# Optimization experiments

Hardware: AMD Instinct MI355X
Metric: run time of the kernel (lower is better)

## Reference

```python
import jax, jax.numpy as jnp
import numpy as np

HID = 64
NUM_LAYER = 3
N_OBJ = 100000
N_P1, N_P2, N_P3 = 200000, 400000, 200000
NUM_GRAPHS = 256


def _mlp(x, w1, b1, w2, b2):
    # pyg.nn.MLP([in, hid, out], norm=None): Linear -> ReLU -> Linear
    return jnp.dot(jax.nn.relu(jnp.dot(x, w1) + b1), w2) + b2


def _gather(obj, ei):
    # ei: [arity, n_atoms] object index per argument slot
    r, n = ei.shape
    g = jnp.take(obj, ei, axis=0)  # [r, n, HID]
    return jnp.moveaxis(g, 0, 1).reshape(n, r * HID)  # concat per-position embeddings


def _scatter(atom, ei, n_obj):
    # split atom embedding [n, r*HID] into r chunks and scatter-add to objects
    r, n = ei.shape
    chunks = jnp.moveaxis(atom.reshape(n, r, HID), 1, 0).reshape(r * n, HID)
    return jax.ops.segment_sum(chunks, ei.reshape(-1), num_segments=n_obj)


def _lin_init(key, fan_in, fan_out):
    kw, kb = jax.random.split(key)
    w = jax.random.normal(kw, (fan_in, fan_out), jnp.float32) / np.float32(np.sqrt(fan_in))
    b = jax.random.normal(kb, (fan_out,), jnp.float32) * 0.01
    return w, b


def setup_inputs() -> dict:
    key = jax.random.key(0)
    ks = jax.random.split(key, 16)
    inp = {}
    inp["x_obj"] = jnp.zeros((N_OBJ, 1), jnp.float32)
    inp["x_p1"] = jnp.zeros((N_P1, 1), jnp.float32)
    inp["x_p2"] = jnp.zeros((N_P2, 2), jnp.float32)
    inp["x_p3"] = jnp.zeros((N_P3, 3), jnp.float32)
    for i, (name, r) in enumerate([("p1", 1), ("p2", 2), ("p3", 3)]):
        d = HID * r
        w1, b1 = _lin_init(ks[2 * i], d, d)
        w2, b2 = _lin_init(ks[2 * i + 1], d, d)
        inp[f"w_{name}_1"], inp[f"b_{name}_1"] = w1, b1
        inp[f"w_{name}_2"], inp[f"b_{name}_2"] = w2, b2
    inp["w_u1"], inp["b_u1"] = _lin_init(ks[6], 2 * HID, 2 * HID)
    inp["w_u2"], inp["b_u2"] = _lin_init(ks[7], 2 * HID, HID)
    inp["w_r1"], inp["b_r1"] = _lin_init(ks[8], HID, 2 * HID)
    inp["w_r2"], inp["b_r2"] = _lin_init(ks[9], 2 * HID, 1)
    inp["ei_p1"] = jax.random.randint(ks[10], (1, N_P1), 0, N_OBJ, jnp.int32)
    inp["ei_p2"] = jax.random.randint(ks[11], (2, N_P2), 0, N_OBJ, jnp.int32)
    inp["ei_p3"] = jax.random.randint(ks[12], (3, N_P3), 0, N_OBJ, jnp.int32)
    inp["batch_obj"] = jnp.sort(jax.random.randint(ks[13], (N_OBJ,), 0, NUM_GRAPHS, jnp.int32))
    inp["num_graphs"] = NUM_GRAPHS
    return inp


def reference(x_obj, x_p1, x_p2, x_p3,
              w_p1_1, b_p1_1, w_p1_2, b_p1_2,
              w_p2_1, b_p2_1, w_p2_2, b_p2_2,
              w_p3_1, b_p3_1, w_p3_2, b_p3_2,
              w_u1, b_u1, w_u2, b_u2,
              w_r1, b_r1, w_r2, b_r2,
              ei_p1, ei_p2, ei_p3, batch_obj, num_graphs):
    n_obj = x_obj.shape[0]
    # encoding_layer: everything starts at zeros of size [N, F*hidden]
    obj = jnp.zeros((n_obj, x_obj.shape[1] * HID), jnp.float32)
    for _ in range(NUM_LAYER):
        # FanOutMP: gather arg-object embeddings, per-predicate MLP -> atom embeddings
        a1 = _mlp(_gather(obj, ei_p1), w_p1_1, b_p1_1, w_p1_2, b_p1_2)
        a2 = _mlp(_gather(obj, ei_p2), w_p2_1, b_p2_1, w_p2_2, b_p2_2)
        a3 = _mlp(_gather(obj, ei_p3), w_p3_1, b_p3_1, w_p3_2, b_p3_2)
        # FanInMP: split atom emb into arity chunks, scatter-add back to objects
        agg = (_scatter(a1, ei_p1, n_obj) + _scatter(a2, ei_p2, n_obj)
               + _scatter(a3, ei_p3, n_obj))
        # obj_update on cat([old_obj, aggregated])
        obj = _mlp(jnp.concatenate([obj, agg], axis=1), w_u1, b_u1, w_u2, b_u2)
    # global_add_pool + readout
    pooled = jax.ops.segment_sum(obj, batch_obj, num_segments=num_graphs)
    return _mlp(pooled, w_r1, b_r1, w_r2, b_r2).reshape(-1)
```

## Files before the change

### kernel.cpp

```cpp
#include <hip/hip_runtime.h>

typedef _Float16 h8 __attribute__((ext_vector_type(8)));
typedef _Float16 h4 __attribute__((ext_vector_type(4)));
typedef float f32x4 __attribute__((ext_vector_type(4)));

__device__ __forceinline__ f32x4 mfma3(h8 ah, h8 al, h8 bh, h8 bl, f32x4 c) {
    c = __builtin_amdgcn_mfma_f32_16x16x32_f16(ah, bh, c, 0, 0, 0);
    c = __builtin_amdgcn_mfma_f32_16x16x32_f16(ah, bl, c, 0, 0, 0);
    c = __builtin_amdgcn_mfma_f32_16x16x32_f16(al, bh, c, 0, 0, 0);
    return c;
}

__launch_bounds__(256)
__global__ void wprep(const float* __restrict__ w_p1_1, const float* __restrict__ w_p1_2,
                      const float* __restrict__ w_p2_1, const float* __restrict__ w_p2_2,
                      const float* __restrict__ w_p3_1, const float* __restrict__ w_p3_2,
                      const float* __restrict__ w_u1, const float* __restrict__ w_u2,
                      _Float16* __restrict__ hb)
{
    int b = blockIdx.x;
    const float* src; int K, N, base; size_t off;
    if      (b < 16)  { src = w_p1_1; K = 64;  N = 64;  base = 0;   off = 0;      }
    else if (b < 32)  { src = w_p1_2; K = 64;  N = 64;  base = 16;  off = 8192;   }
    else if (b < 96)  { src = w_p2_1; K = 128; N = 128; base = 32;  off = 16384;  }
    else if (b < 160) { src = w_p2_2; K = 128; N = 128; base = 96;  off = 49152;  }
    else if (b < 304) { src = w_p3_1; K = 192; N = 192; base = 160; off = 81920;  }
    else if (b < 448) { src = w_p3_2; K = 192; N = 192; base = 304; off = 155648; }
    else if (b < 512) { src = w_u1;   K = 128; N = 128; base = 448; off = 229376; }
    else              { src = w_u2;   K = 128; N = 64;  base = 512; off = 262144; }
    int e = (b - base) * 256 + threadIdx.x;
    if (e < K * N) {
        int n = e / K, k = e - n * K;
        float x = src[k * N + n];
        _Float16 h = (_Float16)x;
        hb[off + e] = h;
        hb[off + (size_t)K * N + e] = (_Float16)(x - (float)h);
    }
}

__launch_bounds__(256)
__global__ void aconst_k(const float* __restrict__ b_p1_1, const float* __restrict__ w_p1_2,
                         const float* __restrict__ b_p1_2,
                         const float* __restrict__ b_p2_1, const float* __restrict__ w_p2_2,
                         const float* __restrict__ b_p2_2,
                         const float* __restrict__ b_p3_1, const float* __restrict__ w_p3_2,
                         const float* __restrict__ b_p3_2,
                         float* __restrict__ ac)
{
    int p = blockIdx.x;
    const float *b1, *w2, *b2; int D, off;
    if      (p == 0) { b1 = b_p1_1; w2 = w_p1_2; b2 = b_p1_2; D = 64;  off = 0;   }
    else if (p == 1) { b1 = b_p2_1; w2 = w_p2_2; b2 = b_p2_2; D = 128; off = 64;  }
    else             { b1 = b_p3_1; w2 = w_p3_2; b2 = b_p3_2; D = 192; off = 192; }
    int n = threadIdx.x;
    if (n < D) {
        float s = b2[n];
        for (int k = 0; k < D; ++k) {
            float h = b1[k];
            h = h > 0.f ? h : 0.f;
            s = fmaf(h, w2[k * D + n], s);
        }
        ac[off + n] = s;
    }
}

__launch_bounds__(256)
__global__ void hist_k(const int* __restrict__ ei1, const int* __restrict__ ei2,
                       const int* __restrict__ ei3, int* __restrict__ counts,
                       int n_obj, int n1, int n2, int n3)
{
    int e = blockIdx.x * 256 + threadIdx.x;
    int t1 = n1, t2 = n1 + 2 * n2, t3 = t2 + 3 * n3;
    if (e < t1) {
        atomicAdd(&counts[ei1[e]], 1);
    } else if (e < t2) {
        int x = e - t1; int slot = x / n2;
        atomicAdd(&counts[(size_t)(1 + slot) * n_obj + ei2[x]], 1);
    } else if (e < t3) {
        int x = e - t2; int slot = x / n3;
        atomicAdd(&counts[(size_t)(3 + slot) * n_obj + ei3[x]], 1);
    }
}

__launch_bounds__(256)
__global__ void bcast_k(const int* __restrict__ counts, const float* __restrict__ ac,
                        float* __restrict__ agg, int n_obj)
{
    __shared__ float ch[384];
    int tid = threadIdx.x;
    for (int i = tid; i < 384; i += 256) ch[i] = ac[i];
    __syncthreads();
    int i = blockIdx.x * 256 + tid;
    int o = i >> 4, q = i & 15;
    if (o < n_obj) {
        float c[6];
#pragma unroll
        for (int j = 0; j < 6; ++j) c[j] = (float)counts[(size_t)j * n_obj + o];
        float4 v;
        float* vp = (float*)&v;
#pragma unroll
        for (int comp = 0; comp < 4; ++comp) {
            int col = 4 * q + comp;
            float s = 0.f;
#pragma unroll
            for (int j = 0; j < 6; ++j) s = fmaf(c[j], ch[j * 64 + col], s);
            vp[comp] = s;
        }
        ((float4*)agg)[(size_t)o * 16 + q] = v;
    }
}

template<int R>
__device__ __forceinline__ void pred_body(
    char* smem,
    const float* __restrict__ obj, const int* __restrict__ ei,
    const _Float16* __restrict__ W1h, const _Float16* __restrict__ W1l,
    const float* __restrict__ B1,
    const _Float16* __restrict__ W2h, const _Float16* __restrict__ W2l,
    const float* __restrict__ B2,
    float* __restrict__ agg, int n_atoms, int blk)
{
    constexpr int D = 64 * R;
    constexpr int KC = D / 32;
    constexpr int LDA = D + 8;
    _Float16* Ah = (_Float16*)smem;
    _Float16* Al = Ah + 64 * LDA;
    int* eis = (int*)(Al + 64 * LDA);

    const int tid = threadIdx.x;
    const int wave = tid >> 6, lane = tid & 63;
    const int r = lane & 15, g = lane >> 4;
    const int a_base = blk * 64;
    const int tb = wave * R;

    for (int i = tid; i < R * 64; i += 256) {
        int s = i >> 6, a = i & 63;
        int ag = a_base + a; if (ag >= n_atoms) ag = n_atoms - 1;
        eis[i] = ei[s * n_atoms + ag];
    }
    __syncthreads();
    {
        const float4* obj4 = (const float4*)obj;
        float4 vv[4 * R];
#pragma unroll
        for (int i = 0; i < 4 * R; ++i) {
            int f = tid + 256 * i;
            int a = f / (R * 16), rem = f % (R * 16);
            int s = rem >> 4, q = rem & 15;
            vv[i] = obj4[(size_t)eis[s * 64 + a] * 16 + q];
        }
#pragma unroll
        for (int i = 0; i < 4 * R; ++i) {
            int f = tid + 256 * i;
            int a = f / (R * 16), rem = f % (R * 16);
            int s = rem >> 4, q = rem & 15;
            float4 v = vv[i];
            _Float16 h0 = (_Float16)v.x, h1 = (_Float16)v.y,
                     h2 = (_Float16)v.z, h3 = (_Float16)v.w;
            h4 hv = {h0, h1, h2, h3};
            h4 lv = {(_Float16)(v.x - (float)h0), (_Float16)(v.y - (float)h1),
                     (_Float16)(v.z - (float)h2), (_Float16)(v.w - (float)h3)};
            *(h4*)(Ah + a * LDA + s * 64 + 4 * q) = hv;
            *(h4*)(Al + a * LDA + s * 64 + 4 * q) = lv;
        }
    }
    __syncthreads();

    f32x4 z = {0.f, 0.f, 0.f, 0.f};
    f32x4 acc[4][R];
#pragma unroll
    for (int rt = 0; rt < 4; ++rt)
#pragma unroll
        for (int t = 0; t < R; ++t) acc[rt][t] = z;

    {
        h8 bh[2][R], bl[2][R];
#pragma unroll
        for (int t = 0; t < R; ++t) {
            size_t wo = (size_t)((tb + t) * 16 + r) * D + g * 8;
            bh[0][t] = *(const h8*)(W1h + wo);
            bl[0][t] = *(const h8*)(W1l + wo);
        }
#pragma unroll
        for (int kc = 0; kc < KC; ++kc) {
            const int cur = kc & 1, nxt = cur ^ 1;
            if (kc + 1 < KC) {
#pragma unroll
                for (int t = 0; t < R; ++t) {
                    size_t wo = (size_t)((tb + t) * 16 + r) * D + (kc + 1) * 32 + g * 8;
                    bh[nxt][t] = *(const h8*)(W1h + wo);
                    bl[nxt][t] = *(const h8*)(W1l + wo);
                }
            }
            const int ko = kc * 32 + g * 8;
            h8 ah[4], al[4];
#pragma unroll
            for (int rt = 0; rt < 4; ++rt) {
                ah[rt] = *(const h8*)(Ah + (rt * 16 + r) * LDA + ko);
                al[rt] = *(const h8*)(Al + (rt * 16 + r) * LDA + ko);
            }
#pragma unroll
            for (int t = 0; t < R; ++t)
#pragma unroll
                for (int rt = 0; rt < 4; ++rt)
                    acc[rt][t] = mfma3(ah[rt], al[rt], bh[cur][t], bl[cur][t], acc[rt][t]);
        }
    }
    __syncthreads();

#pragma unroll
    for (int t = 0; t < R; ++t) {
        int col = (tb + t) * 16 + r;
        float b1 = B1[col];
#pragma unroll
        for (int rt = 0; rt < 4; ++rt)
#pragma unroll
            for (int q = 0; q < 4; ++q) {
                int row = rt * 16 + g * 4 + q;
                float h = acc[rt][t][q] + b1;
                h = h > 0.f ? h : 0.f;
                _Float16 hh = (_Float16)h;
                Ah[row * LDA + col] = hh;
                Al[row * LDA + col] = (_Float16)(h - (float)hh);
            }
    }
    __syncthreads();

#pragma unroll
    for (int rt = 0; rt < 4; ++rt)
#pragma unroll
        for (int t = 0; t < R; ++t) acc[rt][t] = z;
    {
        h8 bh[2][R], bl[2][R];
#pragma unroll
        for (int t = 0; t < R; ++t) {
            size_t wo = (size_t)((tb + t) * 16 + r) * D + g * 8;
            bh[0][t] = *(const h8*)(W2h + wo);
            bl[0][t] = *(const h8*)(W2l + wo);
        }
#pragma unroll
        for (int kc = 0; kc < KC; ++kc) {
            const int cur = kc & 1, nxt = cur ^ 1;
            if (kc + 1 < KC) {
#pragma unroll
                for (int t = 0; t < R; ++t) {
                    size_t wo = (size_t)((tb + t) * 16 + r) * D + (kc + 1) * 32 + g * 8;
                    bh[nxt][t] = *(const h8*)(W2h + wo);
                    bl[nxt][t] = *(const h8*)(W2l + wo);
                }
            }
            const int ko = kc * 32 + g * 8;
            h8 ah[4], al[4];
#pragma unroll
            for (int rt = 0; rt < 4; ++rt) {
                ah[rt] = *(const h8*)(Ah + (rt * 16 + r) * LDA + ko);
                al[rt] = *(const h8*)(Al + (rt * 16 + r) * LDA + ko);
            }
#pragma unroll
            for (int t = 0; t < R; ++t)
#pragma unroll
                for (int rt = 0; rt < 4; ++rt)
                    acc[rt][t] = mfma3(ah[rt], al[rt], bh[cur][t], bl[cur][t], acc[rt][t]);
        }
    }

#pragma unroll
    for (int t = 0; t < R; ++t) {
        int col = (tb + t) * 16 + r;
        float b2 = B2[col];
        int s = col >> 6, cc = col & 63;
#pragma unroll
        for (int rt = 0; rt < 4; ++rt)
#pragma unroll
            for (int q = 0; q < 4; ++q) {
                int row = rt * 16 + g * 4 + q;
                int atom = a_base + row;
                if (atom < n_atoms)
                    atomicAdd(agg + (size_t)eis[s * 64 + row] * 64 + cc,
                              acc[rt][t][q] + b2);
            }
    }
}

__launch_bounds__(256, 3)
__global__ void pred_all(const float* __restrict__ obj, float* __restrict__ agg,
                         const int* __restrict__ ei1, const int* __restrict__ ei2,
                         const int* __restrict__ ei3,
                         const _Float16* __restrict__ hb,
                         const float* __restrict__ b_p1_1, const float* __restrict__ b_p1_2,
                         const float* __restrict__ b_p2_1, const float* __restrict__ b_p2_2,
                         const float* __restrict__ b_p3_1, const float* __restrict__ b_p3_2,
                         int n1, int n2, int n3, int nb3, int nb2)
{
    extern __shared__ char smem[];
    int b = blockIdx.x;
    if (b < nb3) {
        pred_body<3>(smem, obj, ei3, hb + 81920, hb + 118784, b_p3_1,
                     hb + 155648, hb + 192512, b_p3_2, agg, n3, b);
    } else if (b < nb3 + nb2) {
        pred_body<2>(smem, obj, ei2, hb + 16384, hb + 32768, b_p2_1,
                     hb + 49152, hb + 65536, b_p2_2, agg, n2, b - nb3);
    } else {
        pred_body<1>(smem, obj, ei1, hb + 0, hb + 4096, b_p1_1,
                     hb + 8192, hb + 12288, b_p1_2, agg, n1, b - nb3 - nb2);
    }
}

template<int FIRST>
__launch_bounds__(256, 4)
__global__ void update_mfma(float* __restrict__ obj, float* __restrict__ agg,
                            const _Float16* __restrict__ W1h, const _Float16* __restrict__ W1l,
                            const float* __restrict__ B1,
                            const _Float16* __restrict__ W2h, const _Float16* __restrict__ W2l,
                            const float* __restrict__ B2,
                            int n_obj, int zero_agg)
{
    constexpr int LDA = 136;
    __shared__ _Float16 Ah[64 * LDA];
    __shared__ _Float16 Al[64 * LDA];

    const int tid = threadIdx.x;
    const int wave = tid >> 6, lane = tid & 63;
    const int r = lane & 15, g = lane >> 4;
    const int a_base = blockIdx.x * 64;

    {
        const float4* o4 = (const float4*)obj;
        const float4* g4 = (const float4*)agg;
#pragma unroll
        for (int i = 0; i < 8; ++i) {
            int f = tid + 256 * i;
            int a = f >> 5, q = f & 31;
            int rg = a_base + a; if (rg >= n_obj) rg = n_obj - 1;
            float4 v;
            if (FIRST && q < 16) {
                v = make_float4(0.f, 0.f, 0.f, 0.f);
            } else {
                v = (q < 16) ? o4[(size_t)rg * 16 + q] : g4[(size_t)rg * 16 + (q - 16)];
            }
            _Float16 h0 = (_Float16)v.x, h1 = (_Float16)v.y,
                     h2 = (_Float16)v.z, h3 = (_Float16)v.w;
            h4 hv = {h0, h1, h2, h3};
            h4 lv = {(_Float16)(v.x - (float)h0), (_Float16)(v.y - (float)h1),
                     (_Float16)(v.z - (float)h2), (_Float16)(v.w - (float)h3)};
            *(h4*)(Ah + a * LDA + 4 * q) = hv;
            *(h4*)(Al + a * LDA + 4 * q) = lv;
        }
    }
    __syncthreads();

    f32x4 z = {0.f, 0.f, 0.f, 0.f};
    f32x4 acc[4][2];
#pragma unroll
    for (int rt = 0; rt < 4; ++rt) { acc[rt][0] = z; acc[rt][1] = z; }
    {
        h8 bh[2][2], bl[2][2];
#pragma unroll
        for (int t = 0; t < 2; ++t) {
            size_t wo = (size_t)((wave * 2 + t) * 16 + r) * 128 + g * 8;
            bh[0][t] = *(const h8*)(W1h + wo);
            bl[0][t] = *(const h8*)(W1l + wo);
        }
#pragma unroll
        for (int kc = 0; kc < 4; ++kc) {
            const int cur = kc & 1, nxt = cur ^ 1;
            if (kc + 1 < 4) {
#pragma unroll
                for (int t = 0; t < 2; ++t) {
                    size_t wo = (size_t)((wave * 2 + t) * 16 + r) * 128 + (kc + 1) * 32 + g * 8;
                    bh[nxt][t] = *(const h8*)(W1h + wo);
                    bl[nxt][t] = *(const h8*)(W1l + wo);
                }
            }
            const int ko = kc * 32 + g * 8;
            h8 ah[4], al[4];
#pragma unroll
            for (int rt = 0; rt < 4; ++rt) {
                ah[rt] = *(const h8*)(Ah + (rt * 16 + r) * LDA + ko);
                al[rt] = *(const h8*)(Al + (rt * 16 + r) * LDA + ko);
            }
#pragma unroll
            for (int t = 0; t < 2; ++t)
#pragma unroll
                for (int rt = 0; rt < 4; ++rt)
                    acc[rt][t] = mfma3(ah[rt], al[rt], bh[cur][t], bl[cur][t], acc[rt][t]);
        }
    }
    __syncthreads();
#pragma unroll
    for (int t = 0; t < 2; ++t) {
        int col = (wave * 2 + t) * 16 + r;
        float b1 = B1[col];
#pragma unroll
        for (int rt = 0; rt < 4; ++rt)
#pragma unroll
            for (int q = 0; q < 4; ++q) {
                int row = rt * 16 + g * 4 + q;
                float h = acc[rt][t][q] + b1;
                h = h > 0.f ? h : 0.f;
                _Float16 hh = (_Float16)h;
                Ah[row * LDA + col] = hh;
                Al[row * LDA + col] = (_Float16)(h - (float)hh);
            }
    }
    __syncthreads();

    f32x4 acc2[4];
#pragma unroll
    for (int rt = 0; rt < 4; ++rt) acc2[rt] = z;
    {
        h8 bh[2], bl[2];
        {
            size_t wo = (size_t)(wave * 16 + r) * 128 + g * 8;
            bh[0] = *(const h8*)(W2h + wo);
            bl[0] = *(const h8*)(W2l + wo);
        }
#pragma unroll
        for (int kc = 0; kc < 4; ++kc) {
            const int cur = kc & 1, nxt = cur ^ 1;
            if (kc + 1 < 4) {
                size_t wo = (size_t)(wave * 16 + r) * 128 + (kc + 1) * 32 + g * 8;
                bh[nxt] = *(const h8*)(W2h + wo);
                bl[nxt] = *(const h8*)(W2l + wo);
            }
            const int ko = kc * 32 + g * 8;
#pragma unroll
            for (int rt = 0; rt < 4; ++rt) {
                h8 ah = *(const h8*)(Ah + (rt * 16 + r) * LDA + ko);
                h8 al = *(const h8*)(Al + (rt * 16 + r) * LDA + ko);
                acc2[rt] = mfma3(ah, al, bh[cur], bl[cur], acc2[rt]);
            }
        }
    }
    {
        int col = wave * 16 + r;
        float b2 = B2[col];
#pragma unroll
        for (int rt = 0; rt < 4; ++rt)
#pragma unroll
            for (int q = 0; q < 4; ++q) {
                int row = a_base + rt * 16 + g * 4 + q;
                if (row < n_obj)
                    obj[(size_t)row * 64 + col] = acc2[rt][q] + b2;
            }
    }
    if (zero_agg) {
        float4 zz = make_float4(0.f, 0.f, 0.f, 0.f);
#pragma unroll
        for (int i = 0; i < 4; ++i) {
            int f = tid + 256 * i;
            int a = f >> 4, q = f & 15;
            int rg = a_base + a;
            if (rg < n_obj) ((float4*)agg)[(size_t)rg * 16 + q] = zz;
        }
    }
}

__global__ void pool_kernel(const float* __restrict__ obj, const int* __restrict__ batch,
                            float* __restrict__ pooled, int n_obj)
{
    int i = blockIdx.x * 256 + threadIdx.x;
    int row = i >> 4, q = i & 15;
    if (row < n_obj) {
        float4 v = ((const float4*)obj)[(size_t)row * 16 + q];
        int g = batch[row];
        float* p = pooled + g * 64 + 4 * q;
        atomicAdd(p + 0, v.x);
        atomicAdd(p + 1, v.y);
        atomicAdd(p + 2, v.z);
        atomicAdd(p + 3, v.w);
    }
}

__launch_bounds__(128)
__global__ void readout_kernel(const float* __restrict__ pooled,
                               const float* __restrict__ w1, const float* __restrict__ b1,
                               const float* __restrict__ w2, const float* __restrict__ b2,
                               float* __restrict__ out)
{
    int g = blockIdx.x, c = threadIdx.x;
    __shared__ float xs[64];
    __shared__ float red[2];
    if (c < 64) xs[c] = pooled[g * 64 + c];
    __syncthreads();
    float h = b1[c];
#pragma unroll
    for (int k = 0; k < 64; ++k) h = fmaf(xs[k], w1[k * 128 + c], h);
    float v = fmaxf(h, 0.f) * w2[c];
#pragma unroll
    for (int off = 32; off > 0; off >>= 1) v += __shfl_down(v, off);
    if ((c & 63) == 0) red[c >> 6] = v;
    __syncthreads();
    if (c == 0) out[g] = red[0] + red[1] + b2[0];
}

extern "C" void kernel_launch(void* const* d_in, const int* in_sizes, int n_in,
                              void* d_out, int out_size, void* d_ws, size_t ws_size,
                              hipStream_t stream)
{
    const float* w_p1_1 = (const float*)d_in[4];
    const float* b_p1_1 = (const float*)d_in[5];
    const float* w_p1_2 = (const float*)d_in[6];
    const float* b_p1_2 = (const float*)d_in[7];
    const float* w_p2_1 = (const float*)d_in[8];
    const float* b_p2_1 = (const float*)d_in[9];
    const float* w_p2_2 = (const float*)d_in[10];
    const float* b_p2_2 = (const float*)d_in[11];
    const float* w_p3_1 = (const float*)d_in[12];
    const float* b_p3_1 = (const float*)d_in[13];
    const float* w_p3_2 = (const float*)d_in[14];
    const float* b_p3_2 = (const float*)d_in[15];
    const float* w_u1 = (const float*)d_in[16];
    const float* b_u1 = (const float*)d_in[17];
    const float* w_u2 = (const float*)d_in[18];
    const float* b_u2 = (const float*)d_in[19];
    const float* w_r1 = (const float*)d_in[20];
    const float* b_r1 = (const float*)d_in[21];
    const float* w_r2 = (const float*)d_in[22];
    const float* b_r2 = (const float*)d_in[23];
    const int* ei_p1 = (const int*)d_in[24];
    const int* ei_p2 = (const int*)d_in[25];
    const int* ei_p3 = (const int*)d_in[26];
    const int* batch = (const int*)d_in[27];

    const int n_obj = in_sizes[0];
    const int n_p1 = in_sizes[24];
    const int n_p2 = in_sizes[25] / 2;
    const int n_p3 = in_sizes[26] / 3;

    float* obj = (float*)d_ws;
    float* agg = obj + (size_t)n_obj * 64;
    float* pooled = agg + (size_t)n_obj * 64;
    _Float16* hb = (_Float16*)(pooled + (size_t)out_size * 64);
    float* endf = (float*)(hb + 278528);
    int* counts = (int*)obj;
    float* ac = (float*)(counts + 6 * (size_t)n_obj);

    const int nb3 = (n_p3 + 63) / 64, nb2 = (n_p2 + 63) / 64, nb1 = (n_p1 + 63) / 64;
    const int pred_smem = 2 * 64 * (192 + 8) * 2 + 3 * 64 * 4;
    (void)endf; (void)ws_size;

    wprep<<<544, 256, 0, stream>>>(w_p1_1, w_p1_2, w_p2_1, w_p2_2, w_p3_1, w_p3_2,
                                   w_u1, w_u2, hb);
    aconst_k<<<3, 256, 0, stream>>>(b_p1_1, w_p1_2, b_p1_2, b_p2_1, w_p2_2, b_p2_2,
                                    b_p3_1, w_p3_2, b_p3_2, ac);
    hipMemsetAsync(counts, 0, 6 * (size_t)n_obj * sizeof(int), stream);
    {
        int tot = n_p1 + 2 * n_p2 + 3 * n_p3;
        hist_k<<<(tot + 255) / 256, 256, 0, stream>>>(ei_p1, ei_p2, ei_p3, counts,
                                                      n_obj, n_p1, n_p2, n_p3);
    }
    bcast_k<<<((size_t)n_obj * 16 + 255) / 256, 256, 0, stream>>>(counts, ac, agg, n_obj);
    update_mfma<1><<<(n_obj + 63) / 64, 256, 0, stream>>>(
        obj, agg, hb + 229376, hb + 245760, b_u1, hb + 262144, hb + 270336, b_u2,
        n_obj, 1);
    for (int l = 1; l < 3; ++l) {
        pred_all<<<nb3 + nb2 + nb1, 256, pred_smem, stream>>>(
            obj, agg, ei_p1, ei_p2, ei_p3, hb,
            b_p1_1, b_p1_2, b_p2_1, b_p2_2, b_p3_1, b_p3_2,
            n_p1, n_p2, n_p3, nb3, nb2);
        update_mfma<0><<<(n_obj + 63) / 64, 256, 0, stream>>>(
            obj, agg, hb + 229376, hb + 245760, b_u1, hb + 262144, hb + 270336, b_u2,
            n_obj, l < 2 ? 1 : 0);
    }
    hipMemsetAsync(pooled, 0, (size_t)out_size * 64 * sizeof(float), stream);
    pool_kernel<<<((size_t)n_obj * 16 + 255) / 256, 256, 0, stream>>>(obj, batch, pooled, n_obj);
    readout_kernel<<<out_size, 128, 0, stream>>>(pooled, w_r1, b_r1, w_r2, b_r2, (float*)d_out);
}
```

Before: 1.413 ms.

## Store object embeddings in fp16 and drop activation low-part MFMA term

Object embeddings are now kept in a half-precision buffer, and activations are no longer split into high and low fp16 parts. The third MFMA per step, which multiplied the activation's low part, is removed. The change halves gather traffic and LDS footprint in the predicate kernel and raises its occupancy target from 3 to 6 blocks. The last update writes fp32 results into the agg buffer for pooling. The cost is accuracy: activations and hidden states are rounded to fp16, so the result may drift from the fp32 reference.

```diff
diff --git a/kernel.cpp b/kernel.cpp
--- a/kernel.cpp
+++ b/kernel.cpp
@@ -4,10 +4,9 @@
 typedef _Float16 h4 __attribute__((ext_vector_type(4)));
 typedef float f32x4 __attribute__((ext_vector_type(4)));
 
-__device__ __forceinline__ f32x4 mfma3(h8 ah, h8 al, h8 bh, h8 bl, f32x4 c) {
+__device__ __forceinline__ f32x4 mfma2(h8 ah, h8 bh, h8 bl, f32x4 c) {
     c = __builtin_amdgcn_mfma_f32_16x16x32_f16(ah, bh, c, 0, 0, 0);
     c = __builtin_amdgcn_mfma_f32_16x16x32_f16(ah, bl, c, 0, 0, 0);
-    c = __builtin_amdgcn_mfma_f32_16x16x32_f16(al, bh, c, 0, 0, 0);
     return c;
 }
 
@@ -113,7 +112,7 @@
 template<int R>
 __device__ __forceinline__ void pred_body(
     char* smem,
-    const float* __restrict__ obj, const int* __restrict__ ei,
+    const _Float16* __restrict__ objh, const int* __restrict__ ei,
     const _Float16* __restrict__ W1h, const _Float16* __restrict__ W1l,
     const float* __restrict__ B1,
     const _Float16* __restrict__ W2h, const _Float16* __restrict__ W2l,
@@ -124,8 +123,7 @@
     constexpr int KC = D / 32;
     constexpr int LDA = D + 8;
     _Float16* Ah = (_Float16*)smem;
-    _Float16* Al = Ah + 64 * LDA;
-    int* eis = (int*)(Al + 64 * LDA);
+    int* eis = (int*)(Ah + 64 * LDA);
 
     const int tid = threadIdx.x;
     const int wave = tid >> 6, lane = tid & 63;
@@ -140,28 +138,20 @@
     }
     __syncthreads();
     {
-        const float4* obj4 = (const float4*)obj;
-        float4 vv[4 * R];
-#pragma unroll
-        for (int i = 0; i < 4 * R; ++i) {
+        h8 vv[2 * R];
+#pragma unroll
+        for (int i = 0; i < 2 * R; ++i) {
             int f = tid + 256 * i;
-            int a = f / (R * 16), rem = f % (R * 16);
-            int s = rem >> 4, q = rem & 15;
-            vv[i] = obj4[(size_t)eis[s * 64 + a] * 16 + q];
-        }
-#pragma unroll
-        for (int i = 0; i < 4 * R; ++i) {
+            int rowslot = f >> 3, c = f & 7;
+            int s = rowslot >> 6, a = rowslot & 63;
+            vv[i] = *(const h8*)(objh + (size_t)eis[s * 64 + a] * 64 + c * 8);
+        }
+#pragma unroll
+        for (int i = 0; i < 2 * R; ++i) {
             int f = tid + 256 * i;
-            int a = f / (R * 16), rem = f % (R * 16);
-            int s = rem >> 4, q = rem & 15;
-            float4 v = vv[i];
-            _Float16 h0 = (_Float16)v.x, h1 = (_Float16)v.y,
-                     h2 = (_Float16)v.z, h3 = (_Float16)v.w;
-            h4 hv = {h0, h1, h2, h3};
-            h4 lv = {(_Float16)(v.x - (float)h0), (_Float16)(v.y - (float)h1),
-                     (_Float16)(v.z - (float)h2), (_Float16)(v.w - (float)h3)};
-            *(h4*)(Ah + a * LDA + s * 64 + 4 * q) = hv;
-            *(h4*)(Al + a * LDA + s * 64 + 4 * q) = lv;
+            int rowslot = f >> 3, c = f & 7;
+            int s = rowslot >> 6, a = rowslot & 63;
+            *(h8*)(Ah + a * LDA + s * 64 + c * 8) = vv[i];
         }
     }
     __syncthreads();
@@ -193,17 +183,15 @@
                 }
             }
             const int ko = kc * 32 + g * 8;
-            h8 ah[4], al[4];
-#pragma unroll
-            for (int rt = 0; rt < 4; ++rt) {
+            h8 ah[4];
+#pragma unroll
+            for (int rt = 0; rt < 4; ++rt)
                 ah[rt] = *(const h8*)(Ah + (rt * 16 + r) * LDA + ko);
-                al[rt] = *(const h8*)(Al + (rt * 16 + r) * LDA + ko);
-            }
 #pragma unroll
             for (int t = 0; t < R; ++t)
 #pragma unroll
                 for (int rt = 0; rt < 4; ++rt)
-                    acc[rt][t] = mfma3(ah[rt], al[rt], bh[cur][t], bl[cur][t], acc[rt][t]);
+                    acc[rt][t] = mfma2(ah[rt], bh[cur][t], bl[cur][t], acc[rt][t]);
         }
     }
     __syncthreads();
@@ -219,9 +207,7 @@
                 int row = rt * 16 + g * 4 + q;
                 float h = acc[rt][t][q] + b1;
                 h = h > 0.f ? h : 0.f;
-                _Float16 hh = (_Float16)h;
-                Ah[row * LDA + col] = hh;
-                Al[row * LDA + col] = (_Float16)(h - (float)hh);
+                Ah[row * LDA + col] = (_Float16)h;
             }
     }
     __syncthreads();
@@ -250,17 +236,15 @@
                 }
             }
             const int ko = kc * 32 + g * 8;
-            h8 ah[4], al[4];
-#pragma unroll
-            for (int rt = 0; rt < 4; ++rt) {
+            h8 ah[4];
+#pragma unroll
+            for (int rt = 0; rt < 4; ++rt)
                 ah[rt] = *(const h8*)(Ah + (rt * 16 + r) * LDA + ko);
-                al[rt] = *(const h8*)(Al + (rt * 16 + r) * LDA + ko);
-            }
 #pragma unroll
             for (int t = 0; t < R; ++t)
 #pragma unroll
                 for (int rt = 0; rt < 4; ++rt)
-                    acc[rt][t] = mfma3(ah[rt], al[rt], bh[cur][t], bl[cur][t], acc[rt][t]);
+                    acc[rt][t] = mfma2(ah[rt], bh[cur][t], bl[cur][t], acc[rt][t]);
         }
     }
 
@@ -282,8 +266,8 @@
     }
 }
 
-__launch_bounds__(256, 3)
-__global__ void pred_all(const float* __restrict__ obj, float* __restrict__ agg,
+__launch_bounds__(256, 6)
+__global__ void pred_all(const _Float16* __restrict__ objh, float* __restrict__ agg,
                          const int* __restrict__ ei1, const int* __restrict__ ei2,
                          const int* __restrict__ ei3,
                          const _Float16* __restrict__ hb,
@@ -295,29 +279,28 @@
     extern __shared__ char smem[];
     int b = blockIdx.x;
     if (b < nb3) {
-        pred_body<3>(smem, obj, ei3, hb + 81920, hb + 118784, b_p3_1,
+        pred_body<3>(smem, objh, ei3, hb + 81920, hb + 118784, b_p3_1,
                      hb + 155648, hb + 192512, b_p3_2, agg, n3, b);
     } else if (b < nb3 + nb2) {
-        pred_body<2>(smem, obj, ei2, hb + 16384, hb + 32768, b_p2_1,
+        pred_body<2>(smem, objh, ei2, hb + 16384, hb + 32768, b_p2_1,
                      hb + 49152, hb + 65536, b_p2_2, agg, n2, b - nb3);
     } else {
-        pred_body<1>(smem, obj, ei1, hb + 0, hb + 4096, b_p1_1,
+        pred_body<1>(smem, objh, ei1, hb + 0, hb + 4096, b_p1_1,
                      hb + 8192, hb + 12288, b_p1_2, agg, n1, b - nb3 - nb2);
     }
 }
 
 template<int FIRST>
 __launch_bounds__(256, 4)
-__global__ void update_mfma(float* __restrict__ obj, float* __restrict__ agg,
+__global__ void update_mfma(_Float16* __restrict__ objh, float* __restrict__ agg,
                             const _Float16* __restrict__ W1h, const _Float16* __restrict__ W1l,
                             const float* __restrict__ B1,
                             const _Float16* __restrict__ W2h, const _Float16* __restrict__ W2l,
                             const float* __restrict__ B2,
-                            int n_obj, int zero_agg)
+                            int n_obj, int zero_agg, int last)
 {
     constexpr int LDA = 136;
     __shared__ _Float16 Ah[64 * LDA];
-    __shared__ _Float16 Al[64 * LDA];
 
     const int tid = threadIdx.x;
     const int wave = tid >> 6, lane = tid & 63;
@@ -325,26 +308,27 @@
     const int a_base = blockIdx.x * 64;
 
     {
-        const float4* o4 = (const float4*)obj;
-        const float4* g4 = (const float4*)agg;
-#pragma unroll
-        for (int i = 0; i < 8; ++i) {
+#pragma unroll
+        for (int i = 0; i < 4; ++i) {
             int f = tid + 256 * i;
-            int a = f >> 5, q = f & 31;
+            int a = f >> 4, c = f & 15;
             int rg = a_base + a; if (rg >= n_obj) rg = n_obj - 1;
-            float4 v;
-            if (FIRST && q < 16) {
-                v = make_float4(0.f, 0.f, 0.f, 0.f);
+            h8 v;
+            if (c < 8) {
+                if (FIRST) {
+                    v = (h8)(_Float16)0.f;
+                } else {
+                    v = *(const h8*)(objh + (size_t)rg * 64 + c * 8);
+                }
             } else {
-                v = (q < 16) ? o4[(size_t)rg * 16 + q] : g4[(size_t)rg * 16 + (q - 16)];
-            }
-            _Float16 h0 = (_Float16)v.x, h1 = (_Float16)v.y,
-                     h2 = (_Float16)v.z, h3 = (_Float16)v.w;
-            h4 hv = {h0, h1, h2, h3};
-            h4 lv = {(_Float16)(v.x - (float)h0), (_Float16)(v.y - (float)h1),
-                     (_Float16)(v.z - (float)h2), (_Float16)(v.w - (float)h3)};
-            *(h4*)(Ah + a * LDA + 4 * q) = hv;
-            *(h4*)(Al + a * LDA + 4 * q) = lv;
+                float4 f0 = ((const float4*)agg)[(size_t)rg * 16 + (c - 8) * 2];
+                float4 f1 = ((const float4*)agg)[(size_t)rg * 16 + (c - 8) * 2 + 1];
+                v[0] = (_Float16)f0.x; v[1] = (_Float16)f0.y;
+                v[2] = (_Float16)f0.z; v[3] = (_Float16)f0.w;
+                v[4] = (_Float16)f1.x; v[5] = (_Float16)f1.y;
+                v[6] = (_Float16)f1.z; v[7] = (_Float16)f1.w;
+            }
+            *(h8*)(Ah + a * LDA + c * 8) = v;
         }
     }
     __syncthreads();
@@ -373,17 +357,15 @@
                 }
             }
             const int ko = kc * 32 + g * 8;
-            h8 ah[4], al[4];
-#pragma unroll
-            for (int rt = 0; rt < 4; ++rt) {
+            h8 ah[4];
+#pragma unroll
+            for (int rt = 0; rt < 4; ++rt)
                 ah[rt] = *(const h8*)(Ah + (rt * 16 + r) * LDA + ko);
-                al[rt] = *(const h8*)(Al + (rt * 16 + r) * LDA + ko);
-            }
 #pragma unroll
             for (int t = 0; t < 2; ++t)
 #pragma unroll
                 for (int rt = 0; rt < 4; ++rt)
-                    acc[rt][t] = mfma3(ah[rt], al[rt], bh[cur][t], bl[cur][t], acc[rt][t]);
+                    acc[rt][t] = mfma2(ah[rt], bh[cur][t], bl[cur][t], acc[rt][t]);
         }
     }
     __syncthreads();
@@ -398,9 +380,7 @@
                 int row = rt * 16 + g * 4 + q;
                 float h = acc[rt][t][q] + b1;
                 h = h > 0.f ? h : 0.f;
-                _Float16 hh = (_Float16)h;
-                Ah[row * LDA + col] = hh;
-                Al[row * LDA + col] = (_Float16)(h - (float)hh);
+                Ah[row * LDA + col] = (_Float16)h;
             }
     }
     __syncthreads();
@@ -427,11 +407,11 @@
 #pragma unroll
             for (int rt = 0; rt < 4; ++rt) {
                 h8 ah = *(const h8*)(Ah + (rt * 16 + r) * LDA + ko);
-                h8 al = *(const h8*)(Al + (rt * 16 + r) * LDA + ko);
-                acc2[rt] = mfma3(ah, al, bh[cur], bl[cur], acc2[rt]);
-            }
-        }
-    }
+                acc2[rt] = mfma2(ah, bh[cur], bl[cur], acc2[rt]);
+            }
+        }
+    }
+    __syncthreads();
     {
         int col = wave * 16 + r;
         float b2 = B2[col];
@@ -440,8 +420,14 @@
 #pragma unroll
             for (int q = 0; q < 4; ++q) {
                 int row = a_base + rt * 16 + g * 4 + q;
-                if (row < n_obj)
-                    obj[(size_t)row * 64 + col] = acc2[rt][q] + b2;
+                if (row < n_obj) {
+                    float v = acc2[rt][q] + b2;
+                    if (last) {
+                        agg[(size_t)row * 64 + col] = v;
+                    } else {
+                        objh[(size_t)row * 64 + col] = (_Float16)v;
+                    }
+                }
             }
     }
     if (zero_agg) {
@@ -528,17 +514,16 @@
     const int n_p2 = in_sizes[25] / 2;
     const int n_p3 = in_sizes[26] / 3;
 
-    float* obj = (float*)d_ws;
-    float* agg = obj + (size_t)n_obj * 64;
+    _Float16* objh = (_Float16*)d_ws;
+    float* agg = (float*)(objh + (size_t)n_obj * 64);
     float* pooled = agg + (size_t)n_obj * 64;
     _Float16* hb = (_Float16*)(pooled + (size_t)out_size * 64);
-    float* endf = (float*)(hb + 278528);
-    int* counts = (int*)obj;
+    int* counts = (int*)objh;
     float* ac = (float*)(counts + 6 * (size_t)n_obj);
 
     const int nb3 = (n_p3 + 63) / 64, nb2 = (n_p2 + 63) / 64, nb1 = (n_p1 + 63) / 64;
-    const int pred_smem = 2 * 64 * (192 + 8) * 2 + 3 * 64 * 4;
-    (void)endf; (void)ws_size;
+    const int pred_smem = 64 * (192 + 8) * 2 + 3 * 64 * 4;
+    (void)ws_size;
 
     wprep<<<544, 256, 0, stream>>>(w_p1_1, w_p1_2, w_p2_1, w_p2_2, w_p3_1, w_p3_2,
                                    w_u1, w_u2, hb);
@@ -552,18 +537,18 @@
     }
     bcast_k<<<((size_t)n_obj * 16 + 255) / 256, 256, 0, stream>>>(counts, ac, agg, n_obj);
     update_mfma<1><<<(n_obj + 63) / 64, 256, 0, stream>>>(
-        obj, agg, hb + 229376, hb + 245760, b_u1, hb + 262144, hb + 270336, b_u2,
-        n_obj, 1);
+        objh, agg, hb + 229376, hb + 245760, b_u1, hb + 262144, hb + 270336, b_u2,
+        n_obj, 1, 0);
     for (int l = 1; l < 3; ++l) {
         pred_all<<<nb3 + nb2 + nb1, 256, pred_smem, stream>>>(
-            obj, agg, ei_p1, ei_p2, ei_p3, hb,
+            objh, agg, ei_p1, ei_p2, ei_p3, hb,
             b_p1_1, b_p1_2, b_p2_1, b_p2_2, b_p3_1, b_p3_2,
             n_p1, n_p2, n_p3, nb3, nb2);
         update_mfma<0><<<(n_obj + 63) / 64, 256, 0, stream>>>(
-            obj, agg, hb + 229376, hb + 245760, b_u1, hb + 262144, hb + 270336, b_u2,
-            n_obj, l < 2 ? 1 : 0);
+            objh, agg, hb + 229376, hb + 245760, b_u1, hb + 262144, hb + 270336, b_u2,
+            n_obj, l < 2 ? 1 : 0, l == 2 ? 1 : 0);
     }
     hipMemsetAsync(pooled, 0, (size_t)out_size * 64 * sizeof(float), stream);
-    pool_kernel<<<((size_t)n_obj * 16 + 255) / 256, 256, 0, stream>>>(obj, batch, pooled, n_obj);
+    pool_kernel<<<((size_t)n_obj * 16 + 255) / 256, 256, 0, stream>>>(agg, batch, pooled, n_obj);
     readout_kernel<<<out_size, 128, 0, stream>>>(pooled, w_r1, b_r1, w_r2, b_r2, (float*)d_out);
 }
```

Measured after the change: 1.326 ms. -6.1%, faster.
